# Kernel optimization log

Measured on AMD Instinct MI355X. Metric: run time of the kernel, lower is better.

The kernel has to match this reference:

```python
import jax, jax.numpy as jnp
import numpy as np

N = 100000
E = 1600000
G = 512  # number of graphs for pooling


def gcn_conv(x, W, b, src, dst, n):
    # PyG GCNConv: h = x @ W; symmetric deg^{-1/2} norm; scatter-add to dst; + bias
    h = x @ W                                            # [N, out]
    deg = jax.ops.segment_sum(jnp.ones(dst.shape, h.dtype), dst, num_segments=n)
    dinv = jnp.where(deg > 0, jax.lax.rsqrt(deg), 0.0)   # [N]
    norm = dinv[src] * dinv[dst]                         # [E']
    msg = norm[:, None] * h[src]                         # gather + scale, [E', out]
    out = jax.ops.segment_sum(msg, dst, num_segments=n)  # scatter-add
    return out + b


def setup_inputs() -> dict:
    key = jax.random.key(0)
    ks = jax.random.split(key, 8)
    x = jax.random.normal(ks[0], (N, 128), dtype=jnp.float32)
    edge_index = jax.random.randint(ks[1], (2, E), 0, N, dtype=jnp.int32)
    batch_index = jnp.sort(jax.random.randint(ks[2], (N,), 0, G, dtype=jnp.int32))
    W1 = jax.random.normal(ks[3], (128, 64), dtype=jnp.float32) * 0.1
    b1 = jax.random.normal(ks[4], (64,), dtype=jnp.float32) * 0.1
    W2 = jax.random.normal(ks[5], (64, 16), dtype=jnp.float32) * 0.1
    b2 = jax.random.normal(ks[6], (16,), dtype=jnp.float32) * 0.1
    return {"x": x, "edge_index": edge_index, "batch_index": batch_index,
            "W1": W1, "b1": b1, "W2": W2, "b2": b2}


def reference(x, edge_index, batch_index, W1, b1, W2, b2):
    n = x.shape[0]
    # add self-loops (PyG GCNConv default)
    loops = jnp.arange(n, dtype=edge_index.dtype)
    src = jnp.concatenate([edge_index[0], loops])
    dst = jnp.concatenate([edge_index[1], loops])

    h = jnp.tanh(gcn_conv(x, W1, b1, src, dst, n))
    h = jnp.tanh(gcn_conv(h, W2, b2, src, dst, n))

    # global_mean_pool over batch_index
    sums = jax.ops.segment_sum(h, batch_index, num_segments=G)            # [G, C]
    cnt = jax.ops.segment_sum(jnp.ones((n,), h.dtype), batch_index, num_segments=G)
    pooled = sums / jnp.maximum(cnt, 1.0)[:, None]
    return jax.nn.sigmoid(pooled)
```

## Files before the change

kernel.cpp:

```cpp
#include <hip/hip_runtime.h>
#include <hip/hip_bf16.h>

typedef float f4 __attribute__((ext_vector_type(4)));
typedef unsigned int uint32;
typedef _Float16 h16;
typedef _Float16 h16x2 __attribute__((ext_vector_type(2)));
typedef _Float16 f16x8 __attribute__((ext_vector_type(8)));
typedef float f32x4v __attribute__((ext_vector_type(4)));

union h2u { uint32 u; h16 h[2]; h16x2 v; };

#define BSH 8
#define CHUNK 4096
#define CAP 6144

__global__ __launch_bounds__(256) void bscat_k(const int* __restrict__ src, const int* __restrict__ dst,
                                               int* __restrict__ bcur, unsigned int* __restrict__ bedge,
                                               const int* __restrict__ batch, int* __restrict__ gstart,
                                               int E, int B, int N, int G, int nchunk) {
    int tid = threadIdx.x;
    if (blockIdx.x >= nchunk) {
        int i = (blockIdx.x - nchunk) * 256 + tid;
        if (i >= N) return;
        int b = batch[i];
        int prev = (i == 0) ? -1 : batch[i - 1];
        for (int g = prev + 1; g <= b; ++g) gstart[g] = i;
        if (i == N - 1) {
            for (int g = b + 1; g <= G; ++g) gstart[g] = N;
        }
        return;
    }
    __shared__ int hist[512], lbase[512], cur2[512], gb[512];
    __shared__ int sa[512], sb[512];
    __shared__ unsigned int sedge[CHUNK];
    __shared__ unsigned short posb[CHUNK];
    int base = blockIdx.x * CHUNK;
    int n = min(CHUNK, E - base);
    for (int i = tid; i < 512; i += 256) hist[i] = 0;
    __syncthreads();
    for (int i = tid; i < n; i += 256) atomicAdd(&hist[dst[base + i] >> BSH], 1);
    __syncthreads();
    #pragma unroll
    for (int k = 0; k < 2; ++k) { int i = tid + k * 256; sa[i] = hist[i]; }
    __syncthreads();
    int* c = sa; int* nx = sb;
    for (int off = 1; off < 512; off <<= 1) {
        #pragma unroll
        for (int k = 0; k < 2; ++k) { int i = tid + k * 256; nx[i] = c[i] + (i >= off ? c[i - off] : 0); }
        __syncthreads();
        int* t = c; c = nx; nx = t;
    }
    #pragma unroll
    for (int k = 0; k < 2; ++k) {
        int i = tid + k * 256;
        int ex = c[i] - hist[i];
        lbase[i] = ex; cur2[i] = ex;
        if (i < B) gb[i] = hist[i] ? (i * CAP + atomicAdd(&bcur[i], hist[i])) : 0;
    }
    for (int t = tid; t < B; t += 256) {
        int e0 = lbase[t], e1 = e0 + hist[t];
        for (int j = e0; j < e1; ++j) posb[j] = (unsigned short)t;
    }
    __syncthreads();
    for (int i = tid; i < n; i += 256) {
        int d = dst[base + i];
        int s = src[base + i];
        int b = d >> BSH;
        int p = atomicAdd(&cur2[b], 1);
        sedge[p] = ((unsigned int)s << BSH) | (unsigned int)(d & ((1 << BSH) - 1));
    }
    __syncthreads();
    for (int i = tid; i < n; i += 256) {
        int b = posb[i];
        bedge[gb[b] + (i - lbase[b])] = sedge[i];
    }
}

union SharedU {
    struct { int hist[256], cur2[256], sa[256], sb[256]; int cols[CAP]; } p1;
    struct { h16 xS[64][136]; h16 wS[8192]; } p2;
};

__global__ __launch_bounds__(256) void bcsrgemm_k(const unsigned int* __restrict__ bedge,
                                                  const int* __restrict__ bcur,
                                                  const float* __restrict__ x, const float* __restrict__ W1,
                                                  int* __restrict__ row_ptr, int* __restrict__ cnt,
                                                  float* __restrict__ dinv, int* __restrict__ col,
                                                  h16* __restrict__ hsh, int N, int B) {
    __shared__ SharedU su;
    __shared__ float sdinv[256];
    int b = blockIdx.x, tid = threadIdx.x;
    int node0 = b << BSH;
    int g0 = b * CAP;
    int n = min(bcur[b], CAP);

    su.p1.hist[tid] = 0;
    __syncthreads();
    for (int i = tid; i < n; i += 256) atomicAdd(&su.p1.hist[bedge[g0 + i] & 255], 1);
    __syncthreads();
    su.p1.sa[tid] = su.p1.hist[tid];
    __syncthreads();
    int* c = su.p1.sa; int* nx = su.p1.sb;
    for (int off = 1; off < 256; off <<= 1) {
        nx[tid] = c[tid] + (tid >= off ? c[tid - off] : 0);
        __syncthreads();
        int* t = c; c = nx; nx = t;
    }
    int ex = c[tid] - su.p1.hist[tid];
    su.p1.cur2[tid] = ex;
    int node = node0 + tid;
    {
        int deg = su.p1.hist[tid];
        float di = rsqrtf((float)(deg + 1));
        sdinv[tid] = di;
        if (node < N) {
            cnt[node] = deg;
            row_ptr[node] = g0 + ex;
            dinv[node] = di;
        }
    }
    __syncthreads();
    for (int i = tid; i < n; i += 256) {
        unsigned int e = bedge[g0 + i];
        int p = atomicAdd(&su.p1.cur2[e & 255], 1);
        if (p < CAP) su.p1.cols[p] = (int)(e >> BSH);
    }
    __syncthreads();
    for (int i = tid; i < n; i += 256) col[g0 + i] = (i < CAP) ? su.p1.cols[i] : 0;
    __syncthreads();

    #pragma unroll
    for (int i = 0; i < 32; ++i) {
        int idx = tid + i * 256;
        int k = idx >> 6, cc = idx & 63;
        su.p2.wS[(((k >> 3) * 64) + cc) * 8 + (k & 7)] = (h16)W1[idx];
    }
    const int wv = tid >> 6;
    const int lane = tid & 63;
    const int q = lane >> 4;
    const int cc16 = lane & 15;
    for (int t = 0; t < 4; ++t) {
        int trow0 = node0 + t * 64;
        #pragma unroll
        for (int it = 0; it < 8; ++it) {
            int i = tid + it * 256;
            int r = i >> 5;
            int k4 = (i & 31) * 4;
            int row = trow0 + r;
            f4 v = (f4)(0.0f);
            if (row < N) v = *(const f4*)(x + (size_t)row * 128 + k4);
            su.p2.xS[r][k4 + 0] = (h16)v.x; su.p2.xS[r][k4 + 1] = (h16)v.y;
            su.p2.xS[r][k4 + 2] = (h16)v.z; su.p2.xS[r][k4 + 3] = (h16)v.w;
        }
        __syncthreads();
        f32x4v acc0 = {0.f, 0.f, 0.f, 0.f}, acc1 = acc0, acc2 = acc0, acc3 = acc0;
        #pragma unroll
        for (int kb = 0; kb < 4; ++kb) {
            f16x8 a = *(const f16x8*)&su.p2.xS[wv * 16 + cc16][kb * 32 + q * 8];
            const h16* wb = &su.p2.wS[(size_t)((kb * 4 + q) * 64) * 8];
            f16x8 b0 = *(const f16x8*)&wb[(0 * 16 + cc16) * 8];
            f16x8 b1 = *(const f16x8*)&wb[(1 * 16 + cc16) * 8];
            f16x8 b2 = *(const f16x8*)&wb[(2 * 16 + cc16) * 8];
            f16x8 b3 = *(const f16x8*)&wb[(3 * 16 + cc16) * 8];
            acc0 = __builtin_amdgcn_mfma_f32_16x16x32_f16(a, b0, acc0, 0, 0, 0);
            acc1 = __builtin_amdgcn_mfma_f32_16x16x32_f16(a, b1, acc1, 0, 0, 0);
            acc2 = __builtin_amdgcn_mfma_f32_16x16x32_f16(a, b2, acc2, 0, 0, 0);
            acc3 = __builtin_amdgcn_mfma_f32_16x16x32_f16(a, b3, acc3, 0, 0, 0);
        }
        #pragma unroll
        for (int j = 0; j < 4; ++j) {
            int lrow = t * 64 + wv * 16 + q * 4 + j;
            int row = node0 + lrow;
            if (row < N) {
                float di = sdinv[lrow];
                size_t bo = (size_t)row * 64;
                hsh[bo +  0 + cc16] = (h16)(acc0[j] * di);
                hsh[bo + 16 + cc16] = (h16)(acc1[j] * di);
                hsh[bo + 32 + cc16] = (h16)(acc2[j] * di);
                hsh[bo + 48 + cc16] = (h16)(acc3[j] * di);
            }
        }
        __syncthreads();
    }
}

__global__ __launch_bounds__(256) void agg1_k(const h16* __restrict__ hsh, const int* __restrict__ row_ptr,
                                              const int* __restrict__ cnt, const int* __restrict__ col,
                                              const float* __restrict__ dinv, const float* __restrict__ b1,
                                              const float* __restrict__ W2, h16* __restrict__ h2sh, int N) {
    int wid = blockIdx.x * 4 + (threadIdx.x >> 6);
    int lane = threadIdx.x & 63;
    if (wid >= N) return;
    const int c16 = lane & 15;
    const int hh  = lane >> 4;
    float wreg[16];
    #pragma unroll
    for (int k = 0; k < 16; ++k) wreg[k] = W2[(hh * 16 + k) * 16 + c16];
    float bias = b1[lane];

    const int c2 = lane & 31;
    const int h  = lane >> 5;
    const uint32* rowbase = (const uint32*)hsh + c2;

    int beg = row_ptr[wid];
    int num = cnt[wid];
    float accx = 0.0f, accy = 0.0f;
    for (int e0 = 0; e0 < num; e0 += 64) {
        int rem = num - e0;
        int el = 0;
        if (lane < rem) el = col[beg + e0 + lane];
        int m = rem < 64 ? rem : 64;
        int e = 0;
        for (; e + 16 <= m; e += 16) {
            int s0 = __shfl(el, e + h);
            int s1 = __shfl(el, e + 2 + h);
            int s2 = __shfl(el, e + 4 + h);
            int s3 = __shfl(el, e + 6 + h);
            int s4 = __shfl(el, e + 8 + h);
            int s5 = __shfl(el, e + 10 + h);
            int s6 = __shfl(el, e + 12 + h);
            int s7 = __shfl(el, e + 14 + h);
            h2u u0, u1, u2, u3, u4, u5, u6, u7;
            u0.u = rowbase[(size_t)s0 * 32];
            u1.u = rowbase[(size_t)s1 * 32];
            u2.u = rowbase[(size_t)s2 * 32];
            u3.u = rowbase[(size_t)s3 * 32];
            u4.u = rowbase[(size_t)s4 * 32];
            u5.u = rowbase[(size_t)s5 * 32];
            u6.u = rowbase[(size_t)s6 * 32];
            u7.u = rowbase[(size_t)s7 * 32];
            h16x2 t01 = u0.v + u1.v;
            h16x2 t23 = u2.v + u3.v;
            h16x2 t45 = u4.v + u5.v;
            h16x2 t67 = u6.v + u7.v;
            h16x2 t03 = t01 + t23;
            h16x2 t47 = t45 + t67;
            h16x2 tt  = t03 + t47;
            accx += (float)tt[0];
            accy += (float)tt[1];
        }
        for (; e + 8 <= m; e += 8) {
            int s0 = __shfl(el, e + h);
            int s1 = __shfl(el, e + 2 + h);
            int s2 = __shfl(el, e + 4 + h);
            int s3 = __shfl(el, e + 6 + h);
            h2u u0, u1, u2, u3;
            u0.u = rowbase[(size_t)s0 * 32];
            u1.u = rowbase[(size_t)s1 * 32];
            u2.u = rowbase[(size_t)s2 * 32];
            u3.u = rowbase[(size_t)s3 * 32];
            accx += ((float)u0.h[0] + (float)u1.h[0]) + ((float)u2.h[0] + (float)u3.h[0]);
            accy += ((float)u0.h[1] + (float)u1.h[1]) + ((float)u2.h[1] + (float)u3.h[1]);
        }
        for (; e + 4 <= m; e += 4) {
            int s0 = __shfl(el, e + h);
            int s1 = __shfl(el, e + 2 + h);
            h2u u0, u1;
            u0.u = rowbase[(size_t)s0 * 32];
            u1.u = rowbase[(size_t)s1 * 32];
            accx += (float)u0.h[0] + (float)u1.h[0];
            accy += (float)u0.h[1] + (float)u1.h[1];
        }
        for (; e + 2 <= m; e += 2) {
            int s = __shfl(el, e + h);
            h2u u; u.u = rowbase[(size_t)s * 32];
            accx += (float)u.h[0];
            accy += (float)u.h[1];
        }
        if (e < m) {
            int s = __shfl(el, e);
            if (h == 0) {
                h2u u; u.u = rowbase[(size_t)s * 32];
                accx += (float)u.h[0];
                accy += (float)u.h[1];
            }
        }
    }
    accx += __shfl_xor(accx, 32);
    accy += __shfl_xor(accy, 32);
    float ra = __shfl(accx, lane >> 1);
    float rb = __shfl(accy, lane >> 1);
    float acc = (lane & 1) ? rb : ra;

    float di = dinv[wid];
    float self = (float)hsh[(size_t)wid * 64 + lane];
    float h1v = tanhf(di * (acc + self) + bias);

    float p = 0.0f;
    #pragma unroll
    for (int k = 0; k < 16; ++k) {
        float hv = __shfl(h1v, hh * 16 + k);
        p += hv * wreg[k];
    }
    p += __shfl_xor(p, 16);
    p += __shfl_xor(p, 32);
    if (lane < 16) h2sh[(size_t)wid * 16 + lane] = (h16)(di * p);
}

__global__ __launch_bounds__(256) void agg2_k(const h16* __restrict__ h2sh, const int* __restrict__ row_ptr,
                                              const int* __restrict__ cnt, const int* __restrict__ col,
                                              const float* __restrict__ dinv, const float* __restrict__ b2,
                                              h16* __restrict__ h2h, int N) {
    int t = blockIdx.x * 256 + threadIdx.x;
    int node = t >> 4;
    int c = t & 15;
    int sub = (threadIdx.x >> 4) & 3;
    if (node >= N) return;
    int beg = row_ptr[node];
    int num = cnt[node];
    float acc = 0.0f;
    for (int e0 = 0; e0 < num; e0 += 16) {
        int rem = num - e0;
        int el = 0;
        if (c < rem) el = col[beg + e0 + c];
        int m = rem < 16 ? rem : 16;
        int e = 0;
        for (; e + 4 <= m; e += 4) {
            int s0 = __shfl(el, (sub << 4) + e + 0);
            int s1 = __shfl(el, (sub << 4) + e + 1);
            int s2 = __shfl(el, (sub << 4) + e + 2);
            int s3 = __shfl(el, (sub << 4) + e + 3);
            float v0 = (float)h2sh[(size_t)s0 * 16 + c];
            float v1 = (float)h2sh[(size_t)s1 * 16 + c];
            float v2 = (float)h2sh[(size_t)s2 * 16 + c];
            float v3 = (float)h2sh[(size_t)s3 * 16 + c];
            acc += (v0 + v1) + (v2 + v3);
        }
        for (; e < m; ++e) {
            int s = __shfl(el, (sub << 4) + e);
            acc += (float)h2sh[(size_t)s * 16 + c];
        }
    }
    float di = dinv[node];
    float self = (float)h2sh[(size_t)node * 16 + c];
    h2h[(size_t)node * 16 + c] = (h16)tanhf(di * (acc + self) + b2[c]);
}

__global__ __launch_bounds__(256) void pool_seg_k(const h16* __restrict__ h2h, const int* __restrict__ gstart,
                                                  float* __restrict__ out) {
    __shared__ float sd[16][16];
    int g = blockIdx.x;
    int beg = gstart[g], end = gstart[g + 1];
    int tid = threadIdx.x;
    int c = tid & 15, r = tid >> 4;
    float acc = 0.0f;
    for (int i = beg + r; i < end; i += 16)
        acc += (float)h2h[(size_t)i * 16 + c];
    sd[r][c] = acc;
    __syncthreads();
    if (r < 8) sd[r][c] += sd[r + 8][c];
    __syncthreads();
    if (r < 4) sd[r][c] += sd[r + 4][c];
    __syncthreads();
    if (r < 2) sd[r][c] += sd[r + 2][c];
    __syncthreads();
    if (r == 0) {
        float m = (sd[0][c] + sd[1][c]) / fmaxf((float)(end - beg), 1.0f);
        out[g * 16 + c] = 1.0f / (1.0f + expf(-m));
    }
}

extern "C" void kernel_launch(void* const* d_in, const int* in_sizes, int n_in,
                              void* d_out, int out_size, void* d_ws, size_t ws_size,
                              hipStream_t stream) {
    const float* x     = (const float*)d_in[0];
    const int*   ei    = (const int*)d_in[1];
    const int*   batch = (const int*)d_in[2];
    const float* W1    = (const float*)d_in[3];
    const float* b1    = (const float*)d_in[4];
    const float* W2    = (const float*)d_in[5];
    const float* b2    = (const float*)d_in[6];
    float* out = (float*)d_out;

    const int N = in_sizes[2];
    const int E = in_sizes[1] / 2;
    const int G = out_size / 16;
    const int* src = ei;
    const int* dst = ei + E;

    const int B = (N + 255) >> 8;
    const int nchunk = (E + CHUNK - 1) / CHUNK;
    const int nbound = (N + 255) / 256;

    char* w = (char*)d_ws;
    int*   bcur     = (int*)w;    w += 512 * 4;
    int*   row_ptr  = (int*)w;    w += (size_t)N * 4;
    int*   cnt      = (int*)w;    w += (size_t)N * 4;
    float* dinv     = (float*)w;  w += (size_t)N * 4;
    int*   gstart   = (int*)w;    w += 528 * 4;
    int*   col      = (int*)w;    w += (size_t)B * CAP * 4;
    h16*   hsh      = (h16*)w;    w += (size_t)N * 64 * 2;
    h16*   h2sh     = (h16*)w;    w += (size_t)N * 16 * 2;
    h16*   h2h      = (h16*)w;    w += (size_t)N * 16 * 2;
    unsigned int* bedge = (unsigned int*)w;  w += (size_t)B * CAP * 4;

    hipMemsetAsync(bcur, 0, 512 * 4, stream);

    bscat_k   <<<nchunk + nbound, 256, 0, stream>>>(src, dst, bcur, bedge, batch, gstart, E, B, N, G, nchunk);
    bcsrgemm_k<<<B, 256, 0, stream>>>(bedge, bcur, x, W1, row_ptr, cnt, dinv, col, hsh, N, B);

    agg1_k  <<<(N + 3) / 4, 256, 0, stream>>>(hsh, row_ptr, cnt, col, dinv, b1, W2, h2sh, N);
    agg2_k  <<<((size_t)N * 16 + 255) / 256, 256, 0, stream>>>(h2sh, row_ptr, cnt, col, dinv, b2, h2h, N);
    pool_seg_k<<<G, 256, 0, stream>>>(h2h, gstart, out);
}
```

Before: 140.6 us.

## Split layer-1 aggregation into two channel-half passes over separate feature arrays

Stores the first-layer transformed features as two 32-channel half arrays and runs the gather-aggregation in two kernels, each over one half. The working set each pass gathers from is halved (6.4 MB instead of 12.8 MB), which is meant to raise cache hit rates for random neighbor gathers. The cost is reading the CSR indices twice, an extra launch, and writing then re-reading an intermediate h1 buffer for the first half.

After: 177.6 us. +26.4%, slower.

```diff
diff --git a/kernel.cpp b/kernel.cpp
--- a/kernel.cpp
+++ b/kernel.cpp
@@ -86,7 +86,7 @@
                                                   const float* __restrict__ x, const float* __restrict__ W1,
                                                   int* __restrict__ row_ptr, int* __restrict__ cnt,
                                                   float* __restrict__ dinv, int* __restrict__ col,
-                                                  h16* __restrict__ hsh, int N, int B) {
+                                                  h16* __restrict__ hshA, h16* __restrict__ hshB, int N, int B) {
     __shared__ SharedU su;
     __shared__ float sdinv[256];
     int b = blockIdx.x, tid = threadIdx.x;
@@ -173,34 +173,27 @@
             int row = node0 + lrow;
             if (row < N) {
                 float di = sdinv[lrow];
-                size_t bo = (size_t)row * 64;
-                hsh[bo +  0 + cc16] = (h16)(acc0[j] * di);
-                hsh[bo + 16 + cc16] = (h16)(acc1[j] * di);
-                hsh[bo + 32 + cc16] = (h16)(acc2[j] * di);
-                hsh[bo + 48 + cc16] = (h16)(acc3[j] * di);
+                size_t boA = (size_t)row * 32;
+                hshA[boA +  0 + cc16] = (h16)(acc0[j] * di);
+                hshA[boA + 16 + cc16] = (h16)(acc1[j] * di);
+                hshB[boA +  0 + cc16] = (h16)(acc2[j] * di);
+                hshB[boA + 16 + cc16] = (h16)(acc3[j] * di);
             }
         }
         __syncthreads();
     }
 }
 
-__global__ __launch_bounds__(256) void agg1_k(const h16* __restrict__ hsh, const int* __restrict__ row_ptr,
-                                              const int* __restrict__ cnt, const int* __restrict__ col,
-                                              const float* __restrict__ dinv, const float* __restrict__ b1,
-                                              const float* __restrict__ W2, h16* __restrict__ h2sh, int N) {
+__global__ __launch_bounds__(256) void agg1a_k(const h16* __restrict__ hshA, const int* __restrict__ row_ptr,
+                                               const int* __restrict__ cnt, const int* __restrict__ col,
+                                               const float* __restrict__ dinv, const float* __restrict__ b1,
+                                               h16* __restrict__ h1h, int N) {
     int wid = blockIdx.x * 4 + (threadIdx.x >> 6);
     int lane = threadIdx.x & 63;
     if (wid >= N) return;
-    const int c16 = lane & 15;
-    const int hh  = lane >> 4;
-    float wreg[16];
-    #pragma unroll
-    for (int k = 0; k < 16; ++k) wreg[k] = W2[(hh * 16 + k) * 16 + c16];
-    float bias = b1[lane];
-
-    const int c2 = lane & 31;
-    const int h  = lane >> 5;
-    const uint32* rowbase = (const uint32*)hsh + c2;
+    const int cp = lane & 15;
+    const int g  = lane >> 4;
+    const uint32* rowbase = (const uint32*)hshA + cp;
 
     int beg = row_ptr[wid];
     int num = cnt[wid];
@@ -212,79 +205,109 @@
         int m = rem < 64 ? rem : 64;
         int e = 0;
         for (; e + 16 <= m; e += 16) {
-            int s0 = __shfl(el, e + h);
-            int s1 = __shfl(el, e + 2 + h);
-            int s2 = __shfl(el, e + 4 + h);
-            int s3 = __shfl(el, e + 6 + h);
-            int s4 = __shfl(el, e + 8 + h);
-            int s5 = __shfl(el, e + 10 + h);
-            int s6 = __shfl(el, e + 12 + h);
-            int s7 = __shfl(el, e + 14 + h);
-            h2u u0, u1, u2, u3, u4, u5, u6, u7;
-            u0.u = rowbase[(size_t)s0 * 32];
-            u1.u = rowbase[(size_t)s1 * 32];
-            u2.u = rowbase[(size_t)s2 * 32];
-            u3.u = rowbase[(size_t)s3 * 32];
-            u4.u = rowbase[(size_t)s4 * 32];
-            u5.u = rowbase[(size_t)s5 * 32];
-            u6.u = rowbase[(size_t)s6 * 32];
-            u7.u = rowbase[(size_t)s7 * 32];
-            h16x2 t01 = u0.v + u1.v;
-            h16x2 t23 = u2.v + u3.v;
-            h16x2 t45 = u4.v + u5.v;
-            h16x2 t67 = u6.v + u7.v;
-            h16x2 t03 = t01 + t23;
-            h16x2 t47 = t45 + t67;
-            h16x2 tt  = t03 + t47;
-            accx += (float)tt[0];
-            accy += (float)tt[1];
-        }
-        for (; e + 8 <= m; e += 8) {
-            int s0 = __shfl(el, e + h);
-            int s1 = __shfl(el, e + 2 + h);
-            int s2 = __shfl(el, e + 4 + h);
-            int s3 = __shfl(el, e + 6 + h);
+            int s0 = __shfl(el, e + g);
+            int s1 = __shfl(el, e + 4 + g);
+            int s2 = __shfl(el, e + 8 + g);
+            int s3 = __shfl(el, e + 12 + g);
             h2u u0, u1, u2, u3;
-            u0.u = rowbase[(size_t)s0 * 32];
-            u1.u = rowbase[(size_t)s1 * 32];
-            u2.u = rowbase[(size_t)s2 * 32];
-            u3.u = rowbase[(size_t)s3 * 32];
+            u0.u = rowbase[(size_t)s0 * 16];
+            u1.u = rowbase[(size_t)s1 * 16];
+            u2.u = rowbase[(size_t)s2 * 16];
+            u3.u = rowbase[(size_t)s3 * 16];
             accx += ((float)u0.h[0] + (float)u1.h[0]) + ((float)u2.h[0] + (float)u3.h[0]);
             accy += ((float)u0.h[1] + (float)u1.h[1]) + ((float)u2.h[1] + (float)u3.h[1]);
         }
         for (; e + 4 <= m; e += 4) {
-            int s0 = __shfl(el, e + h);
-            int s1 = __shfl(el, e + 2 + h);
-            h2u u0, u1;
-            u0.u = rowbase[(size_t)s0 * 32];
-            u1.u = rowbase[(size_t)s1 * 32];
-            accx += (float)u0.h[0] + (float)u1.h[0];
-            accy += (float)u0.h[1] + (float)u1.h[1];
-        }
-        for (; e + 2 <= m; e += 2) {
-            int s = __shfl(el, e + h);
-            h2u u; u.u = rowbase[(size_t)s * 32];
+            int s = __shfl(el, e + g);
+            h2u u; u.u = rowbase[(size_t)s * 16];
             accx += (float)u.h[0];
             accy += (float)u.h[1];
         }
-        if (e < m) {
-            int s = __shfl(el, e);
-            if (h == 0) {
-                h2u u; u.u = rowbase[(size_t)s * 32];
-                accx += (float)u.h[0];
-                accy += (float)u.h[1];
-            }
-        }
-    }
-    accx += __shfl_xor(accx, 32);
-    accy += __shfl_xor(accy, 32);
-    float ra = __shfl(accx, lane >> 1);
-    float rb = __shfl(accy, lane >> 1);
-    float acc = (lane & 1) ? rb : ra;
+        if (e + g < m) {
+            int s = __shfl(el, e + g);
+            h2u u; u.u = rowbase[(size_t)s * 16];
+            accx += (float)u.h[0];
+            accy += (float)u.h[1];
+        }
+    }
+    accx += __shfl_xor(accx, 16); accy += __shfl_xor(accy, 16);
+    accx += __shfl_xor(accx, 32); accy += __shfl_xor(accy, 32);
+    int ch = lane & 31;
+    float ra = __shfl(accx, ch >> 1);
+    float rb = __shfl(accy, ch >> 1);
+    float acc = (ch & 1) ? rb : ra;
 
     float di = dinv[wid];
-    float self = (float)hsh[(size_t)wid * 64 + lane];
-    float h1v = tanhf(di * (acc + self) + bias);
+    float self = (float)hshA[(size_t)wid * 32 + ch];
+    float h1v = tanhf(di * (acc + self) + b1[ch]);
+    if (lane < 32) h1h[(size_t)wid * 64 + lane] = (h16)h1v;
+}
+
+__global__ __launch_bounds__(256) void agg1b_k(const h16* __restrict__ hshB, const int* __restrict__ row_ptr,
+                                               const int* __restrict__ cnt, const int* __restrict__ col,
+                                               const float* __restrict__ dinv, const float* __restrict__ b1,
+                                               const float* __restrict__ W2, const h16* __restrict__ h1h,
+                                               h16* __restrict__ h2sh, int N) {
+    int wid = blockIdx.x * 4 + (threadIdx.x >> 6);
+    int lane = threadIdx.x & 63;
+    if (wid >= N) return;
+    const int c16 = lane & 15;
+    const int hh  = lane >> 4;
+    float wreg[16];
+    #pragma unroll
+    for (int k = 0; k < 16; ++k) wreg[k] = W2[(hh * 16 + k) * 16 + c16];
+
+    const int cp = lane & 15;
+    const int g  = lane >> 4;
+    const uint32* rowbase = (const uint32*)hshB + cp;
+
+    int beg = row_ptr[wid];
+    int num = cnt[wid];
+    float accx = 0.0f, accy = 0.0f;
+    for (int e0 = 0; e0 < num; e0 += 64) {
+        int rem = num - e0;
+        int el = 0;
+        if (lane < rem) el = col[beg + e0 + lane];
+        int m = rem < 64 ? rem : 64;
+        int e = 0;
+        for (; e + 16 <= m; e += 16) {
+            int s0 = __shfl(el, e + g);
+            int s1 = __shfl(el, e + 4 + g);
+            int s2 = __shfl(el, e + 8 + g);
+            int s3 = __shfl(el, e + 12 + g);
+            h2u u0, u1, u2, u3;
+            u0.u = rowbase[(size_t)s0 * 16];
+            u1.u = rowbase[(size_t)s1 * 16];
+            u2.u = rowbase[(size_t)s2 * 16];
+            u3.u = rowbase[(size_t)s3 * 16];
+            accx += ((float)u0.h[0] + (float)u1.h[0]) + ((float)u2.h[0] + (float)u3.h[0]);
+            accy += ((float)u0.h[1] + (float)u1.h[1]) + ((float)u2.h[1] + (float)u3.h[1]);
+        }
+        for (; e + 4 <= m; e += 4) {
+            int s = __shfl(el, e + g);
+            h2u u; u.u = rowbase[(size_t)s * 16];
+            accx += (float)u.h[0];
+            accy += (float)u.h[1];
+        }
+        if (e + g < m) {
+            int s = __shfl(el, e + g);
+            h2u u; u.u = rowbase[(size_t)s * 16];
+            accx += (float)u.h[0];
+            accy += (float)u.h[1];
+        }
+    }
+    accx += __shfl_xor(accx, 16); accy += __shfl_xor(accy, 16);
+    accx += __shfl_xor(accx, 32); accy += __shfl_xor(accy, 32);
+    int ch = lane & 31;
+    float ra = __shfl(accx, ch >> 1);
+    float rb = __shfl(accy, ch >> 1);
+    float acc = (ch & 1) ? rb : ra;
+
+    float di = dinv[wid];
+    float self = (float)hshB[(size_t)wid * 32 + ch];
+    float own = tanhf(di * (acc + self) + b1[32 + ch]);
+
+    float h1v = (lane < 32) ? (float)h1h[(size_t)wid * 64 + lane] : own;
 
     float p = 0.0f;
     #pragma unroll
@@ -389,7 +412,9 @@
     float* dinv     = (float*)w;  w += (size_t)N * 4;
     int*   gstart   = (int*)w;    w += 528 * 4;
     int*   col      = (int*)w;    w += (size_t)B * CAP * 4;
-    h16*   hsh      = (h16*)w;    w += (size_t)N * 64 * 2;
+    h16*   hshA     = (h16*)w;    w += (size_t)N * 32 * 2;
+    h16*   hshB     = (h16*)w;    w += (size_t)N * 32 * 2;
+    h16*   h1h      = (h16*)w;    w += (size_t)N * 64 * 2;
     h16*   h2sh     = (h16*)w;    w += (size_t)N * 16 * 2;
     h16*   h2h      = (h16*)w;    w += (size_t)N * 16 * 2;
     unsigned int* bedge = (unsigned int*)w;  w += (size_t)B * CAP * 4;
@@ -397,9 +422,10 @@
     hipMemsetAsync(bcur, 0, 512 * 4, stream);
 
     bscat_k   <<<nchunk + nbound, 256, 0, stream>>>(src, dst, bcur, bedge, batch, gstart, E, B, N, G, nchunk);
-    bcsrgemm_k<<<B, 256, 0, stream>>>(bedge, bcur, x, W1, row_ptr, cnt, dinv, col, hsh, N, B);
-
-    agg1_k  <<<(N + 3) / 4, 256, 0, stream>>>(hsh, row_ptr, cnt, col, dinv, b1, W2, h2sh, N);
+    bcsrgemm_k<<<B, 256, 0, stream>>>(bedge, bcur, x, W1, row_ptr, cnt, dinv, col, hshA, hshB, N, B);
+
+    agg1a_k <<<(N + 3) / 4, 256, 0, stream>>>(hshA, row_ptr, cnt, col, dinv, b1, h1h, N);
+    agg1b_k <<<(N + 3) / 4, 256, 0, stream>>>(hshB, row_ptr, cnt, col, dinv, b1, W2, h1h, h2sh, N);
     agg2_k  <<<((size_t)N * 16 + 255) / 256, 256, 0, stream>>>(h2sh, row_ptr, cnt, col, dinv, b2, h2h, N);
     pool_seg_k<<<G, 256, 0, stream>>>(h2h, gstart, out);
 }
```
